# Performance work log

Measured on AMD Instinct MI355X. Metric: run time of the kernel, lower is better.

## Reference

```python
import jax, jax.numpy as jnp
import numpy as np

N_NODES = 100000
N_EDGES = 1600000
D_IN = 128
D_OUT = 128


def setup_inputs() -> dict:
    key = jax.random.key(0)
    k1, k2, k3, k4, k5 = jax.random.split(key, 5)
    h = jax.random.normal(k1, (N_NODES, D_IN), dtype=jnp.float32)
    src = jax.random.randint(k2, (N_EDGES,), 0, N_NODES, dtype=jnp.int64)
    dst = jax.random.randint(k3, (N_EDGES,), 0, N_NODES, dtype=jnp.int64)
    # Glorot-ish init for linear weights (PyTorch nn.Linear style: [out, in])
    scale = 1.0 / np.sqrt(D_IN)
    W_self = jax.random.uniform(k4, (D_OUT, D_IN), jnp.float32, -scale, scale)
    W_neigh = jax.random.uniform(k5, (D_OUT, D_IN), jnp.float32, -scale, scale)
    b = jnp.zeros((D_OUT,), dtype=jnp.float32)
    return {"h": h, "src": src, "dst": dst, "W_self": W_self,
            "W_neigh": W_neigh, "b": b}


def reference(h, src, dst, W_self, W_neigh, b):
    n_nodes = h.shape[0]
    # neighbor gather + segment-mean over in-neighbors (DGL fn.copy_u + fn.mean)
    msg = h[src]                                            # [E, D_in]
    neigh_sum = jax.ops.segment_sum(msg, dst, num_segments=n_nodes)
    deg = jax.ops.segment_sum(jnp.ones_like(dst, dtype=h.dtype), dst,
                              num_segments=n_nodes)         # [N]
    h_neigh = neigh_sum / jnp.maximum(deg, 1.0)[:, None]    # mean; 0 for isolated
    # SAGEConv mean: fc_self(h) + fc_neigh(h_neigh) + bias
    out = h @ W_self.T + h_neigh @ W_neigh.T + b
    return out
```

## Files before the change

### kernel.cpp

```cpp
#include <hip/hip_runtime.h>
#include <stdint.h>

#define NN 100000
#define NE 1600000
#define DD 128
#define NTILES ((NN + 127) / 128)
#define NB 512
#define CHUNK (NE / NB)
#define NBUCK ((NN + 255) / 256)

typedef __bf16 bf16x8 __attribute__((ext_vector_type(8)));
typedef float f32x4 __attribute__((ext_vector_type(4)));
typedef float f32x2 __attribute__((ext_vector_type(2)));

__device__ __forceinline__ unsigned int f2bf2(float a, float b) {
  union { float f; unsigned u; } x, y;
  x.f = a; y.f = b;
  unsigned ua = x.u + (0x7FFFu + ((x.u >> 16) & 1u));
  unsigned ub = y.u + (0x7FFFu + ((y.u >> 16) & 1u));
  return (ua >> 16) | (ub & 0xFFFF0000u);
}

__global__ __launch_bounds__(256) void zero_kernel(int* __restrict__ p) {
  int t = blockIdx.x * 256 + threadIdx.x;
  if (t < 2 * NBUCK) p[t] = 0;
}

__global__ __launch_bounds__(256) void convert_kernel(
    const float4* __restrict__ hp, uint2* __restrict__ h8,
    uint4* __restrict__ hbf, const int* __restrict__ dst,
    int* __restrict__ ghist) {
  __shared__ int lh[NBUCK];
  int t = threadIdx.x, b = blockIdx.x;
  int gid = b * 256 + t;
  float4 a = hp[2 * gid], c = hp[2 * gid + 1];
  int lo = __builtin_amdgcn_cvt_pk_fp8_f32(a.x, a.y, 0, false);
  lo = __builtin_amdgcn_cvt_pk_fp8_f32(a.z, a.w, lo, true);
  int hi = __builtin_amdgcn_cvt_pk_fp8_f32(c.x, c.y, 0, false);
  hi = __builtin_amdgcn_cvt_pk_fp8_f32(c.z, c.w, hi, true);
  h8[gid] = make_uint2((unsigned)lo, (unsigned)hi);

  uint4 q;
  q.x = f2bf2(a.x, a.y);
  q.y = f2bf2(a.z, a.w);
  q.z = f2bf2(c.x, c.y);
  q.w = f2bf2(c.z, c.w);
  int m = t >> 4, c8 = t & 15;
  int rt = b & 7, kc = c8 >> 2, quad = c8 & 3;
  hbf[(size_t)(b >> 3) * 2048 + (((rt << 2) + kc) << 6) + (quad << 4) + m] = q;

  if (b < NB) {
    for (int i = t; i < NBUCK; i += 256) lh[i] = 0;
    __syncthreads();
    int e0 = b * CHUNK;
    for (int e = e0 + t; e < e0 + CHUNK; e += 256)
      atomicAdd(&lh[dst[e] >> 8], 1);
    __syncthreads();
    for (int i = t; i < NBUCK; i += 256)
      if (lh[i]) atomicAdd(&ghist[i], lh[i]);
  }
}

__global__ __launch_bounds__(256) void coarse_scatter_kernel(
    const int* __restrict__ src, const int* __restrict__ dst,
    const int* __restrict__ ghist, int* __restrict__ gcur,
    unsigned* __restrict__ ebuf) {
  __shared__ int lhp[512];
  __shared__ int gbp[512];
  __shared__ int lbase[NBUCK];
  __shared__ int lcur[NBUCK];
  __shared__ int gstart[NBUCK];
  __shared__ unsigned sdata[CHUNK];
  __shared__ int sgpos[CHUNK];
  int t = threadIdx.x, b = blockIdx.x;
  lhp[t] = 0;
  lhp[t + 256] = 0;
  gbp[t] = (t < NBUCK) ? ghist[t] : 0;
  gbp[t + 256] = (t + 256 < NBUCK) ? ghist[t + 256] : 0;
  __syncthreads();
  int e0 = b * CHUNK;
  for (int e = e0 + t; e < e0 + CHUNK; e += 256)
    atomicAdd(&lhp[dst[e] >> 8], 1);
  __syncthreads();
  int c0 = lhp[t], c1 = lhp[t + 256];
  int g0 = gbp[t], g1 = gbp[t + 256];
  for (int d = 1; d < 512; d <<= 1) {
    int x0 = (t >= d) ? lhp[t - d] : 0;
    int x1 = ((t + 256) >= d) ? lhp[t + 256 - d] : 0;
    int y0 = (t >= d) ? gbp[t - d] : 0;
    int y1 = ((t + 256) >= d) ? gbp[t + 256 - d] : 0;
    __syncthreads();
    lhp[t] += x0; lhp[t + 256] += x1;
    gbp[t] += y0; gbp[t + 256] += y1;
    __syncthreads();
  }
  if (t < NBUCK) {
    lbase[t] = lhp[t] - c0;
    lcur[t] = 0;
    int resv = c0 ? atomicAdd(&gcur[t], c0) : 0;
    gstart[t] = (gbp[t] - g0) + resv;
  }
  int i2 = t + 256;
  if (i2 < NBUCK) {
    lbase[i2] = lhp[i2] - c1;
    lcur[i2] = 0;
    int resv = c1 ? atomicAdd(&gcur[i2], c1) : 0;
    gstart[i2] = (gbp[i2] - g1) + resv;
  }
  __syncthreads();
  for (int e = e0 + t; e < e0 + CHUNK; e += 256) {
    int d = dst[e], s = src[e];
    int bk = d >> 8;
    int slot = atomicAdd(&lcur[bk], 1);
    int lp = lbase[bk] + slot;
    sdata[lp] = ((unsigned)(d & 255) << 24) | (unsigned)s;
    sgpos[lp] = gstart[bk] + slot;
  }
  __syncthreads();
  for (int j = t; j < CHUNK; j += 256) ebuf[sgpos[j]] = sdata[j];
}

__global__ __launch_bounds__(256) void fine_sort_kernel(
    const unsigned* __restrict__ ebuf, const int* __restrict__ ghist,
    int* __restrict__ csr, int* __restrict__ offs) {
  __shared__ int gbp[512];
  __shared__ int hist[256], scn[256], cur[256];
  int t = threadIdx.x, g = blockIdx.x;
  gbp[t] = (t < NBUCK) ? ghist[t] : 0;
  gbp[t + 256] = (t + 256 < NBUCK) ? ghist[t + 256] : 0;
  hist[t] = 0;
  __syncthreads();
  for (int d = 1; d < 512; d <<= 1) {
    int y0 = (t >= d) ? gbp[t - d] : 0;
    int y1 = ((t + 256) >= d) ? gbp[t + 256 - d] : 0;
    __syncthreads();
    gbp[t] += y0; gbp[t + 256] += y1;
    __syncthreads();
  }
  int end = gbp[g];
  int base = end - ghist[g];
  for (int j = base + t; j < end; j += 256)
    atomicAdd(&hist[ebuf[j] >> 24], 1);
  __syncthreads();
  int v = hist[t];
  scn[t] = v;
  __syncthreads();
  for (int d = 1; d < 256; d <<= 1) {
    int x = (t >= d) ? scn[t - d] : 0;
    __syncthreads();
    scn[t] += x;
    __syncthreads();
  }
  int excl = scn[t] - v;
  int node = g * 256 + t;
  if (node < NN) offs[node] = base + excl;
  if (node == NN - 1) offs[NN] = NE;
  cur[t] = excl;
  __syncthreads();
  for (int j = base + t; j < end; j += 256) {
    unsigned p = ebuf[j];
    int pos = atomicAdd(&cur[p >> 24], 1);
    csr[base + pos] = (int)(p & 0x00FFFFFFu);
  }
}

__device__ __forceinline__ void acc16(float* a, uint4 u) {
  f32x2 p;
  p = __builtin_amdgcn_cvt_pk_f32_fp8(u.x, false); a[0] += p.x;  a[1] += p.y;
  p = __builtin_amdgcn_cvt_pk_f32_fp8(u.x, true);  a[2] += p.x;  a[3] += p.y;
  p = __builtin_amdgcn_cvt_pk_f32_fp8(u.y, false); a[4] += p.x;  a[5] += p.y;
  p = __builtin_amdgcn_cvt_pk_f32_fp8(u.y, true);  a[6] += p.x;  a[7] += p.y;
  p = __builtin_amdgcn_cvt_pk_f32_fp8(u.z, false); a[8] += p.x;  a[9] += p.y;
  p = __builtin_amdgcn_cvt_pk_f32_fp8(u.z, true);  a[10] += p.x; a[11] += p.y;
  p = __builtin_amdgcn_cvt_pk_f32_fp8(u.w, false); a[12] += p.x; a[13] += p.y;
  p = __builtin_amdgcn_cvt_pk_f32_fp8(u.w, true);  a[14] += p.x; a[15] += p.y;
}

__global__ __launch_bounds__(256) void gather_frag_kernel(
    const uint4* __restrict__ h8, const int* __restrict__ offs,
    const int* __restrict__ csr, uint4* __restrict__ hfrag) {
  int q = (blockIdx.x * 256 + threadIdx.x) >> 3;
  int l = threadIdx.x & 7;
  float a[16];
#pragma unroll
  for (int i = 0; i < 16; i++) a[i] = 0.f;
  float sc = 0.f;
  if (q < NN) {
    int off0 = offs[q], off1 = offs[q + 1];
    int j = off0;
    for (; j + 4 <= off1; j += 4) {
      int s0 = csr[j], s1 = csr[j + 1], s2 = csr[j + 2], s3 = csr[j + 3];
      uint4 u0 = h8[(size_t)s0 * 8 + l];
      uint4 u1 = h8[(size_t)s1 * 8 + l];
      uint4 u2 = h8[(size_t)s2 * 8 + l];
      uint4 u3 = h8[(size_t)s3 * 8 + l];
      acc16(a, u0); acc16(a, u1); acc16(a, u2); acc16(a, u3);
    }
    for (; j < off1; j++) acc16(a, h8[(size_t)csr[j] * 8 + l]);
    int deg = off1 - off0;
    sc = (deg > 0) ? (1.0f / (float)deg) : 0.0f;
  }
  uint4 r0, r1;
  r0.x = f2bf2(a[0] * sc, a[1] * sc);   r0.y = f2bf2(a[2] * sc, a[3] * sc);
  r0.z = f2bf2(a[4] * sc, a[5] * sc);   r0.w = f2bf2(a[6] * sc, a[7] * sc);
  r1.x = f2bf2(a[8] * sc, a[9] * sc);   r1.y = f2bf2(a[10] * sc, a[11] * sc);
  r1.z = f2bf2(a[12] * sc, a[13] * sc); r1.w = f2bf2(a[14] * sc, a[15] * sc);
  int r = q & 127;
  int rt = r >> 4, m = r & 15;
  int kc = l >> 1, quad = (l & 1) << 1;
  int slot = (((rt << 2) + kc) << 6) + (quad << 4) + m;
  uint4* base = hfrag + (size_t)(q >> 7) * 2048;
  base[slot] = r0;
  base[slot + 16] = r1;
}

__device__ __forceinline__ void stage_w(const float* __restrict__ X,
                                        uint4* buf, int t) {
#pragma unroll
  for (int i = 0; i < 8; i++) {
    int id = t + (i << 8);
    int r = id >> 4;
    int c8 = id & 15;
    const float4* p = (const float4*)(X + (size_t)r * DD + (c8 << 3));
    float4 v0 = p[0], v1 = p[1];
    uint4 q;
    q.x = f2bf2(v0.x, v0.y);
    q.y = f2bf2(v0.z, v0.w);
    q.z = f2bf2(v1.x, v1.y);
    q.w = f2bf2(v1.z, v1.w);
    int rt = r >> 4, m = r & 15, kc = c8 >> 2, quad = c8 & 3;
    buf[(((rt << 2) + kc) << 6) + (quad << 4) + m] = q;
  }
}

__device__ __forceinline__ void compute_reg(const uint4* a, const uint4* sWb,
                                            f32x4 acc[2][8], int lane) {
#pragma unroll
  for (int kc = 0; kc < 4; kc++) {
    bf16x8 bfr[8];
#pragma unroll
    for (int n = 0; n < 8; n++)
      bfr[n] = *(const bf16x8*)&sWb[(((n << 2) + kc) << 6) + lane];
    bf16x8 a0 = *(const bf16x8*)&a[kc];
    bf16x8 a1 = *(const bf16x8*)&a[4 + kc];
#pragma unroll
    for (int n = 0; n < 8; n++) {
      acc[0][n] = __builtin_amdgcn_mfma_f32_16x16x32_bf16(a0, bfr[n], acc[0][n], 0, 0, 0);
      acc[1][n] = __builtin_amdgcn_mfma_f32_16x16x32_bf16(a1, bfr[n], acc[1][n], 0, 0, 0);
    }
  }
}

__global__ __launch_bounds__(256, 2) void gemm_kernel(
    const uint4* __restrict__ hbf, const uint4* __restrict__ hfrag,
    const float* __restrict__ Wself, const float* __restrict__ Wneigh,
    const float* __restrict__ bias, float* __restrict__ out) {
  __shared__ uint4 sW[4096];
  int t = threadIdx.x;
  int wv = t >> 6;
  int lane = t & 63;
  int row0 = blockIdx.x * 128;

  const uint4* fb1 = hbf + (size_t)blockIdx.x * 2048;
  const uint4* fb2 = hfrag + (size_t)blockIdx.x * 2048;
  uint4 a1[8], a2[8];
#pragma unroll
  for (int kc = 0; kc < 4; kc++) {
    int s0 = ((((wv * 2 + 0) << 2) + kc) << 6) + lane;
    int s1 = ((((wv * 2 + 1) << 2) + kc) << 6) + lane;
    a1[kc] = fb1[s0]; a1[4 + kc] = fb1[s1];
    a2[kc] = fb2[s0]; a2[4 + kc] = fb2[s1];
  }

  stage_w(Wself, sW, t);
  stage_w(Wneigh, sW + 2048, t);

  f32x4 acc[2][8];
#pragma unroll
  for (int i = 0; i < 2; i++)
#pragma unroll
    for (int n = 0; n < 8; n++) acc[i][n] = f32x4{0.f, 0.f, 0.f, 0.f};

  __syncthreads();
  compute_reg(a1, sW, acc, lane);
  compute_reg(a2, sW + 2048, acc, lane);

  int col = lane & 15, rq = lane >> 4;
  float bv[8];
#pragma unroll
  for (int n = 0; n < 8; n++) bv[n] = bias[n * 16 + col];
#pragma unroll
  for (int rt = 0; rt < 2; rt++) {
    int rb = row0 + (wv * 2 + rt) * 16 + rq * 4;
#pragma unroll
    for (int r = 0; r < 4; r++) {
      int row = rb + r;
      if (row < NN) {
        float* op = out + (size_t)row * DD + col;
#pragma unroll
        for (int n = 0; n < 8; n++) op[n * 16] = acc[rt][n][r] + bv[n];
      }
    }
  }
}

extern "C" void kernel_launch(void* const* d_in, const int* in_sizes, int n_in,
                              void* d_out, int out_size, void* d_ws, size_t ws_size,
                              hipStream_t stream) {
  const float* h      = (const float*)d_in[0];
  const int*   src    = (const int*)d_in[1];
  const int*   dst    = (const int*)d_in[2];
  const float* Wself  = (const float*)d_in[3];
  const float* Wneigh = (const float*)d_in[4];
  const float* bias   = (const float*)d_in[5];
  float* out = (float*)d_out;

  char* ws = (char*)d_ws;
  unsigned* h8       = (unsigned*)ws;
  unsigned* hbf      = (unsigned*)(ws + 12800000);
  unsigned* hfrag    = (unsigned*)(ws + 38424576);
  unsigned* ebuf     = (unsigned*)(ws + 38424576);
  int*      csr      = (int*)(ws + 64049152);
  int*      offs     = (int*)(ws + 70449152);
  int*      ghist    = (int*)(ws + 70849168);
  int*      gcur     = (int*)(ws + 70850732);

  zero_kernel<<<(2 * NBUCK + 255) / 256, 256, 0, stream>>>(ghist);
  convert_kernel<<<6250, 256, 0, stream>>>((const float4*)h, (uint2*)h8,
                                           (uint4*)hbf, dst, ghist);
  coarse_scatter_kernel<<<NB, 256, 0, stream>>>(src, dst, ghist, gcur, ebuf);
  fine_sort_kernel<<<NBUCK, 256, 0, stream>>>(ebuf, ghist, csr, offs);
  gather_frag_kernel<<<(NTILES * 128) / 32, 256, 0, stream>>>(
      (const uint4*)h8, offs, csr, (uint4*)hfrag);
  gemm_kernel<<<NTILES, 256, 0, stream>>>((const uint4*)hbf, (const uint4*)hfrag,
                                          Wself, Wneigh, bias, out);
}
```

Before: 229.5 us.

## Build CSR via per-node atomic counting and scan, shrink GEMM LDS footprint

```diff
diff --git a/kernel.cpp b/kernel.cpp
--- a/kernel.cpp
+++ b/kernel.cpp
@@ -5,9 +5,8 @@
 #define NE 1600000
 #define DD 128
 #define NTILES ((NN + 127) / 128)
-#define NB 512
-#define CHUNK (NE / NB)
 #define NBUCK ((NN + 255) / 256)
+#define NCNT (NBUCK * 256)
 
 typedef __bf16 bf16x8 __attribute__((ext_vector_type(8)));
 typedef float f32x4 __attribute__((ext_vector_type(4)));
@@ -21,16 +20,14 @@
   return (ua >> 16) | (ub & 0xFFFF0000u);
 }
 
-__global__ __launch_bounds__(256) void zero_kernel(int* __restrict__ p) {
-  int t = blockIdx.x * 256 + threadIdx.x;
-  if (t < 2 * NBUCK) p[t] = 0;
+__global__ __launch_bounds__(256) void zero_kernel(int* __restrict__ cnt) {
+  cnt[blockIdx.x * 256 + threadIdx.x] = 0;
 }
 
 __global__ __launch_bounds__(256) void convert_kernel(
     const float4* __restrict__ hp, uint2* __restrict__ h8,
     uint4* __restrict__ hbf, const int* __restrict__ dst,
-    int* __restrict__ ghist) {
-  __shared__ int lh[NBUCK];
+    int* __restrict__ cnt) {
   int t = threadIdx.x, b = blockIdx.x;
   int gid = b * 256 + t;
   float4 a = hp[2 * gid], c = hp[2 * gid + 1];
@@ -49,119 +46,67 @@
   int rt = b & 7, kc = c8 >> 2, quad = c8 & 3;
   hbf[(size_t)(b >> 3) * 2048 + (((rt << 2) + kc) << 6) + (quad << 4) + m] = q;
 
-  if (b < NB) {
-    for (int i = t; i < NBUCK; i += 256) lh[i] = 0;
-    __syncthreads();
-    int e0 = b * CHUNK;
-    for (int e = e0 + t; e < e0 + CHUNK; e += 256)
-      atomicAdd(&lh[dst[e] >> 8], 1);
-    __syncthreads();
-    for (int i = t; i < NBUCK; i += 256)
-      if (lh[i]) atomicAdd(&ghist[i], lh[i]);
-  }
-}
-
-__global__ __launch_bounds__(256) void coarse_scatter_kernel(
-    const int* __restrict__ src, const int* __restrict__ dst,
-    const int* __restrict__ ghist, int* __restrict__ gcur,
-    unsigned* __restrict__ ebuf) {
-  __shared__ int lhp[512];
-  __shared__ int gbp[512];
-  __shared__ int lbase[NBUCK];
-  __shared__ int lcur[NBUCK];
-  __shared__ int gstart[NBUCK];
-  __shared__ unsigned sdata[CHUNK];
-  __shared__ int sgpos[CHUNK];
-  int t = threadIdx.x, b = blockIdx.x;
-  lhp[t] = 0;
-  lhp[t + 256] = 0;
-  gbp[t] = (t < NBUCK) ? ghist[t] : 0;
-  gbp[t + 256] = (t + 256 < NBUCK) ? ghist[t + 256] : 0;
-  __syncthreads();
-  int e0 = b * CHUNK;
-  for (int e = e0 + t; e < e0 + CHUNK; e += 256)
-    atomicAdd(&lhp[dst[e] >> 8], 1);
-  __syncthreads();
-  int c0 = lhp[t], c1 = lhp[t + 256];
-  int g0 = gbp[t], g1 = gbp[t + 256];
+  atomicAdd(&cnt[dst[gid]], 1);
+}
+
+__global__ __launch_bounds__(256) void blocksum_kernel(const int* __restrict__ cnt,
+                                                       int* __restrict__ bsum) {
+  __shared__ int s[256];
+  int t = threadIdx.x;
+  s[t] = cnt[blockIdx.x * 256 + t];
+  __syncthreads();
+  for (int d = 128; d > 0; d >>= 1) {
+    if (t < d) s[t] += s[t + d];
+    __syncthreads();
+  }
+  if (t == 0) bsum[blockIdx.x] = s[0];
+}
+
+__global__ __launch_bounds__(512) void scanbsum_kernel(const int* __restrict__ bsum,
+                                                       int* __restrict__ bsum_ex) {
+  __shared__ int s[512];
+  int t = threadIdx.x;
+  int v = (t < NBUCK) ? bsum[t] : 0;
+  s[t] = v;
+  __syncthreads();
   for (int d = 1; d < 512; d <<= 1) {
-    int x0 = (t >= d) ? lhp[t - d] : 0;
-    int x1 = ((t + 256) >= d) ? lhp[t + 256 - d] : 0;
-    int y0 = (t >= d) ? gbp[t - d] : 0;
-    int y1 = ((t + 256) >= d) ? gbp[t + 256 - d] : 0;
-    __syncthreads();
-    lhp[t] += x0; lhp[t + 256] += x1;
-    gbp[t] += y0; gbp[t + 256] += y1;
-    __syncthreads();
-  }
-  if (t < NBUCK) {
-    lbase[t] = lhp[t] - c0;
-    lcur[t] = 0;
-    int resv = c0 ? atomicAdd(&gcur[t], c0) : 0;
-    gstart[t] = (gbp[t] - g0) + resv;
-  }
-  int i2 = t + 256;
-  if (i2 < NBUCK) {
-    lbase[i2] = lhp[i2] - c1;
-    lcur[i2] = 0;
-    int resv = c1 ? atomicAdd(&gcur[i2], c1) : 0;
-    gstart[i2] = (gbp[i2] - g1) + resv;
-  }
-  __syncthreads();
-  for (int e = e0 + t; e < e0 + CHUNK; e += 256) {
-    int d = dst[e], s = src[e];
-    int bk = d >> 8;
-    int slot = atomicAdd(&lcur[bk], 1);
-    int lp = lbase[bk] + slot;
-    sdata[lp] = ((unsigned)(d & 255) << 24) | (unsigned)s;
-    sgpos[lp] = gstart[bk] + slot;
-  }
-  __syncthreads();
-  for (int j = t; j < CHUNK; j += 256) ebuf[sgpos[j]] = sdata[j];
-}
-
-__global__ __launch_bounds__(256) void fine_sort_kernel(
-    const unsigned* __restrict__ ebuf, const int* __restrict__ ghist,
-    int* __restrict__ csr, int* __restrict__ offs) {
-  __shared__ int gbp[512];
-  __shared__ int hist[256], scn[256], cur[256];
-  int t = threadIdx.x, g = blockIdx.x;
-  gbp[t] = (t < NBUCK) ? ghist[t] : 0;
-  gbp[t + 256] = (t + 256 < NBUCK) ? ghist[t + 256] : 0;
-  hist[t] = 0;
-  __syncthreads();
-  for (int d = 1; d < 512; d <<= 1) {
-    int y0 = (t >= d) ? gbp[t - d] : 0;
-    int y1 = ((t + 256) >= d) ? gbp[t + 256 - d] : 0;
-    __syncthreads();
-    gbp[t] += y0; gbp[t + 256] += y1;
-    __syncthreads();
-  }
-  int end = gbp[g];
-  int base = end - ghist[g];
-  for (int j = base + t; j < end; j += 256)
-    atomicAdd(&hist[ebuf[j] >> 24], 1);
-  __syncthreads();
-  int v = hist[t];
-  scn[t] = v;
+    int x = (t >= d) ? s[t - d] : 0;
+    __syncthreads();
+    s[t] += x;
+    __syncthreads();
+  }
+  if (t < NBUCK) bsum_ex[t] = s[t] - v;
+}
+
+__global__ __launch_bounds__(256) void scanapply_kernel(const int* __restrict__ cnt,
+                                                        const int* __restrict__ bsum_ex,
+                                                        int* __restrict__ offs,
+                                                        int* __restrict__ cur) {
+  __shared__ int s[256];
+  int t = threadIdx.x;
+  int idx = blockIdx.x * 256 + t;
+  int v = cnt[idx];
+  s[t] = v;
   __syncthreads();
   for (int d = 1; d < 256; d <<= 1) {
-    int x = (t >= d) ? scn[t - d] : 0;
-    __syncthreads();
-    scn[t] += x;
-    __syncthreads();
-  }
-  int excl = scn[t] - v;
-  int node = g * 256 + t;
-  if (node < NN) offs[node] = base + excl;
-  if (node == NN - 1) offs[NN] = NE;
-  cur[t] = excl;
-  __syncthreads();
-  for (int j = base + t; j < end; j += 256) {
-    unsigned p = ebuf[j];
-    int pos = atomicAdd(&cur[p >> 24], 1);
-    csr[base + pos] = (int)(p & 0x00FFFFFFu);
-  }
+    int x = (t >= d) ? s[t - d] : 0;
+    __syncthreads();
+    s[t] += x;
+    __syncthreads();
+  }
+  int excl = bsum_ex[blockIdx.x] + s[t] - v;
+  if (idx < NN) { offs[idx] = excl; cur[idx] = excl; }
+  if (idx == NN - 1) offs[NN] = NE;
+}
+
+__global__ __launch_bounds__(256) void scatter_kernel(const int* __restrict__ src,
+                                                      const int* __restrict__ dst,
+                                                      int* __restrict__ cur,
+                                                      int* __restrict__ csr) {
+  int e = blockIdx.x * 256 + threadIdx.x;
+  int d = dst[e];
+  int pos = atomicAdd(&cur[d], 1);
+  csr[pos] = src[e];
 }
 
 __device__ __forceinline__ void acc16(float* a, uint4 u) {
@@ -251,11 +196,11 @@
   }
 }
 
-__global__ __launch_bounds__(256, 2) void gemm_kernel(
+__global__ __launch_bounds__(256, 4) void gemm_kernel(
     const uint4* __restrict__ hbf, const uint4* __restrict__ hfrag,
     const float* __restrict__ Wself, const float* __restrict__ Wneigh,
     const float* __restrict__ bias, float* __restrict__ out) {
-  __shared__ uint4 sW[4096];
+  __shared__ uint4 sW[2048];
   int t = threadIdx.x;
   int wv = t >> 6;
   int lane = t & 63;
@@ -272,18 +217,19 @@
     a2[kc] = fb2[s0]; a2[4 + kc] = fb2[s1];
   }
 
+  f32x4 acc[2][8];
+#pragma unroll
+  for (int i = 0; i < 2; i++)
+#pragma unroll
+    for (int n = 0; n < 8; n++) acc[i][n] = f32x4{0.f, 0.f, 0.f, 0.f};
+
   stage_w(Wself, sW, t);
-  stage_w(Wneigh, sW + 2048, t);
-
-  f32x4 acc[2][8];
-#pragma unroll
-  for (int i = 0; i < 2; i++)
-#pragma unroll
-    for (int n = 0; n < 8; n++) acc[i][n] = f32x4{0.f, 0.f, 0.f, 0.f};
-
   __syncthreads();
   compute_reg(a1, sW, acc, lane);
-  compute_reg(a2, sW + 2048, acc, lane);
+  __syncthreads();
+  stage_w(Wneigh, sW, t);
+  __syncthreads();
+  compute_reg(a2, sW, acc, lane);
 
   int col = lane & 15, rq = lane >> 4;
   float bv[8];
@@ -319,17 +265,20 @@
   unsigned* h8       = (unsigned*)ws;
   unsigned* hbf      = (unsigned*)(ws + 12800000);
   unsigned* hfrag    = (unsigned*)(ws + 38424576);
-  unsigned* ebuf     = (unsigned*)(ws + 38424576);
   int*      csr      = (int*)(ws + 64049152);
   int*      offs     = (int*)(ws + 70449152);
-  int*      ghist    = (int*)(ws + 70849168);
-  int*      gcur     = (int*)(ws + 70850732);
-
-  zero_kernel<<<(2 * NBUCK + 255) / 256, 256, 0, stream>>>(ghist);
+  int*      cnt      = (int*)(ws + 70849168);
+  int*      cur      = (int*)(ws + 71249552);
+  int*      bsum     = (int*)(ws + 71649936);
+  int*      bsum_ex  = (int*)(ws + 71651504);
+
+  zero_kernel<<<NBUCK, 256, 0, stream>>>(cnt);
   convert_kernel<<<6250, 256, 0, stream>>>((const float4*)h, (uint2*)h8,
-                                           (uint4*)hbf, dst, ghist);
-  coarse_scatter_kernel<<<NB, 256, 0, stream>>>(src, dst, ghist, gcur, ebuf);
-  fine_sort_kernel<<<NBUCK, 256, 0, stream>>>(ebuf, ghist, csr, offs);
+                                           (uint4*)hbf, dst, cnt);
+  blocksum_kernel<<<NBUCK, 256, 0, stream>>>(cnt, bsum);
+  scanbsum_kernel<<<1, 512, 0, stream>>>(bsum, bsum_ex);
+  scanapply_kernel<<<NBUCK, 256, 0, stream>>>(cnt, bsum_ex, offs, cur);
+  scatter_kernel<<<6250, 256, 0, stream>>>(src, dst, cur, csr);
   gather_frag_kernel<<<(NTILES * 128) / 32, 256, 0, stream>>>(
       (const uint4*)h8, offs, csr, (uint4*)hfrag);
   gemm_kernel<<<NTILES, 256, 0, stream>>>((const uint4*)hbf, (const uint4*)hfrag,
```

Result: slower. 365.1 us (+59.1%).

## Fuse fine bucket sort into neighbor gather via shared memory; halve GEMM LDS

Applied to the files above, without the earlier changes.

```diff
diff --git a/kernel.cpp b/kernel.cpp
--- a/kernel.cpp
+++ b/kernel.cpp
@@ -8,6 +8,7 @@
 #define NB 512
 #define CHUNK (NE / NB)
 #define NBUCK ((NN + 255) / 256)
+#define MAXBE 6144
 
 typedef __bf16 bf16x8 __attribute__((ext_vector_type(8)));
 typedef float f32x4 __attribute__((ext_vector_type(4)));
@@ -120,50 +121,6 @@
   for (int j = t; j < CHUNK; j += 256) ebuf[sgpos[j]] = sdata[j];
 }
 
-__global__ __launch_bounds__(256) void fine_sort_kernel(
-    const unsigned* __restrict__ ebuf, const int* __restrict__ ghist,
-    int* __restrict__ csr, int* __restrict__ offs) {
-  __shared__ int gbp[512];
-  __shared__ int hist[256], scn[256], cur[256];
-  int t = threadIdx.x, g = blockIdx.x;
-  gbp[t] = (t < NBUCK) ? ghist[t] : 0;
-  gbp[t + 256] = (t + 256 < NBUCK) ? ghist[t + 256] : 0;
-  hist[t] = 0;
-  __syncthreads();
-  for (int d = 1; d < 512; d <<= 1) {
-    int y0 = (t >= d) ? gbp[t - d] : 0;
-    int y1 = ((t + 256) >= d) ? gbp[t + 256 - d] : 0;
-    __syncthreads();
-    gbp[t] += y0; gbp[t + 256] += y1;
-    __syncthreads();
-  }
-  int end = gbp[g];
-  int base = end - ghist[g];
-  for (int j = base + t; j < end; j += 256)
-    atomicAdd(&hist[ebuf[j] >> 24], 1);
-  __syncthreads();
-  int v = hist[t];
-  scn[t] = v;
-  __syncthreads();
-  for (int d = 1; d < 256; d <<= 1) {
-    int x = (t >= d) ? scn[t - d] : 0;
-    __syncthreads();
-    scn[t] += x;
-    __syncthreads();
-  }
-  int excl = scn[t] - v;
-  int node = g * 256 + t;
-  if (node < NN) offs[node] = base + excl;
-  if (node == NN - 1) offs[NN] = NE;
-  cur[t] = excl;
-  __syncthreads();
-  for (int j = base + t; j < end; j += 256) {
-    unsigned p = ebuf[j];
-    int pos = atomicAdd(&cur[p >> 24], 1);
-    csr[base + pos] = (int)(p & 0x00FFFFFFu);
-  }
-}
-
 __device__ __forceinline__ void acc16(float* a, uint4 u) {
   f32x2 p;
   p = __builtin_amdgcn_cvt_pk_f32_fp8(u.x, false); a[0] += p.x;  a[1] += p.y;
@@ -176,42 +133,84 @@
   p = __builtin_amdgcn_cvt_pk_f32_fp8(u.w, true);  a[14] += p.x; a[15] += p.y;
 }
 
-__global__ __launch_bounds__(256) void gather_frag_kernel(
-    const uint4* __restrict__ h8, const int* __restrict__ offs,
-    const int* __restrict__ csr, uint4* __restrict__ hfrag) {
-  int q = (blockIdx.x * 256 + threadIdx.x) >> 3;
-  int l = threadIdx.x & 7;
-  float a[16];
-#pragma unroll
-  for (int i = 0; i < 16; i++) a[i] = 0.f;
-  float sc = 0.f;
-  if (q < NN) {
-    int off0 = offs[q], off1 = offs[q + 1];
-    int j = off0;
-    for (; j + 4 <= off1; j += 4) {
-      int s0 = csr[j], s1 = csr[j + 1], s2 = csr[j + 2], s3 = csr[j + 3];
+__global__ __launch_bounds__(256) void gather_bucket_kernel(
+    const unsigned* __restrict__ ebuf, const int* __restrict__ ghist,
+    const uint4* __restrict__ h8, uint4* __restrict__ hfrag) {
+  __shared__ int gbp[512];
+  __shared__ int hist[256], st[256], cur[256];
+  __shared__ int ssort[MAXBE];
+  int t = threadIdx.x;
+  int bid = blockIdx.x;
+  int g = bid >> 1, p = bid & 1;
+  gbp[t] = (t < NBUCK) ? ghist[t] : 0;
+  gbp[t + 256] = (t + 256 < NBUCK) ? ghist[t + 256] : 0;
+  hist[t] = 0;
+  __syncthreads();
+  for (int d = 1; d < 512; d <<= 1) {
+    int y0 = (t >= d) ? gbp[t - d] : 0;
+    int y1 = ((t + 256) >= d) ? gbp[t + 256 - d] : 0;
+    __syncthreads();
+    gbp[t] += y0; gbp[t + 256] += y1;
+    __syncthreads();
+  }
+  int end = gbp[g];
+  int base = end - ghist[g];
+  for (int j = base + t; j < end; j += 256)
+    atomicAdd(&hist[ebuf[j] >> 24], 1);
+  __syncthreads();
+  int deg = hist[t];
+  st[t] = deg;
+  __syncthreads();
+  for (int d = 1; d < 256; d <<= 1) {
+    int x = (t >= d) ? st[t - d] : 0;
+    __syncthreads();
+    st[t] += x;
+    __syncthreads();
+  }
+  int start = st[t] - deg;
+  __syncthreads();
+  st[t] = start;
+  cur[t] = start;
+  __syncthreads();
+  for (int j = base + t; j < end; j += 256) {
+    unsigned e = ebuf[j];
+    int pos = atomicAdd(&cur[e >> 24], 1);
+    ssort[pos] = (int)(e & 0x00FFFFFFu);
+  }
+  __syncthreads();
+  int grp = t >> 3, l = t & 7;
+#pragma unroll 1
+  for (int k = 0; k < 4; k++) {
+    int r = grp * 4 + k;
+    int ln = p * 128 + r;
+    int j = st[ln];
+    int jend = j + hist[ln];
+    float a[16];
+#pragma unroll
+    for (int i = 0; i < 16; i++) a[i] = 0.f;
+    for (; j + 4 <= jend; j += 4) {
+      int s0 = ssort[j], s1 = ssort[j + 1], s2 = ssort[j + 2], s3 = ssort[j + 3];
       uint4 u0 = h8[(size_t)s0 * 8 + l];
       uint4 u1 = h8[(size_t)s1 * 8 + l];
       uint4 u2 = h8[(size_t)s2 * 8 + l];
       uint4 u3 = h8[(size_t)s3 * 8 + l];
       acc16(a, u0); acc16(a, u1); acc16(a, u2); acc16(a, u3);
     }
-    for (; j < off1; j++) acc16(a, h8[(size_t)csr[j] * 8 + l]);
-    int deg = off1 - off0;
-    sc = (deg > 0) ? (1.0f / (float)deg) : 0.0f;
-  }
-  uint4 r0, r1;
-  r0.x = f2bf2(a[0] * sc, a[1] * sc);   r0.y = f2bf2(a[2] * sc, a[3] * sc);
-  r0.z = f2bf2(a[4] * sc, a[5] * sc);   r0.w = f2bf2(a[6] * sc, a[7] * sc);
-  r1.x = f2bf2(a[8] * sc, a[9] * sc);   r1.y = f2bf2(a[10] * sc, a[11] * sc);
-  r1.z = f2bf2(a[12] * sc, a[13] * sc); r1.w = f2bf2(a[14] * sc, a[15] * sc);
-  int r = q & 127;
-  int rt = r >> 4, m = r & 15;
-  int kc = l >> 1, quad = (l & 1) << 1;
-  int slot = (((rt << 2) + kc) << 6) + (quad << 4) + m;
-  uint4* base = hfrag + (size_t)(q >> 7) * 2048;
-  base[slot] = r0;
-  base[slot + 16] = r1;
+    for (; j < jend; j++) acc16(a, h8[(size_t)ssort[j] * 8 + l]);
+    int dg = hist[ln];
+    float sc = (dg > 0) ? (1.0f / (float)dg) : 0.0f;
+    uint4 r0, r1;
+    r0.x = f2bf2(a[0] * sc, a[1] * sc);   r0.y = f2bf2(a[2] * sc, a[3] * sc);
+    r0.z = f2bf2(a[4] * sc, a[5] * sc);   r0.w = f2bf2(a[6] * sc, a[7] * sc);
+    r1.x = f2bf2(a[8] * sc, a[9] * sc);   r1.y = f2bf2(a[10] * sc, a[11] * sc);
+    r1.z = f2bf2(a[12] * sc, a[13] * sc); r1.w = f2bf2(a[14] * sc, a[15] * sc);
+    int rt = r >> 4, m = r & 15;
+    int kc = l >> 1, quad = (l & 1) << 1;
+    int slot = (((rt << 2) + kc) << 6) + (quad << 4) + m;
+    uint4* bp = hfrag + (size_t)bid * 2048;
+    bp[slot] = r0;
+    bp[slot + 16] = r1;
+  }
 }
 
 __device__ __forceinline__ void stage_w(const float* __restrict__ X,
@@ -251,11 +250,11 @@
   }
 }
 
-__global__ __launch_bounds__(256, 2) void gemm_kernel(
+__global__ __launch_bounds__(256, 4) void gemm_kernel(
     const uint4* __restrict__ hbf, const uint4* __restrict__ hfrag,
     const float* __restrict__ Wself, const float* __restrict__ Wneigh,
     const float* __restrict__ bias, float* __restrict__ out) {
-  __shared__ uint4 sW[4096];
+  __shared__ uint4 sW[2048];
   int t = threadIdx.x;
   int wv = t >> 6;
   int lane = t & 63;
@@ -272,18 +271,19 @@
     a2[kc] = fb2[s0]; a2[4 + kc] = fb2[s1];
   }
 
+  f32x4 acc[2][8];
+#pragma unroll
+  for (int i = 0; i < 2; i++)
+#pragma unroll
+    for (int n = 0; n < 8; n++) acc[i][n] = f32x4{0.f, 0.f, 0.f, 0.f};
+
   stage_w(Wself, sW, t);
-  stage_w(Wneigh, sW + 2048, t);
-
-  f32x4 acc[2][8];
-#pragma unroll
-  for (int i = 0; i < 2; i++)
-#pragma unroll
-    for (int n = 0; n < 8; n++) acc[i][n] = f32x4{0.f, 0.f, 0.f, 0.f};
-
   __syncthreads();
   compute_reg(a1, sW, acc, lane);
-  compute_reg(a2, sW + 2048, acc, lane);
+  __syncthreads();
+  stage_w(Wneigh, sW, t);
+  __syncthreads();
+  compute_reg(a2, sW, acc, lane);
 
   int col = lane & 15, rq = lane >> 4;
   float bv[8];
@@ -319,19 +319,16 @@
   unsigned* h8       = (unsigned*)ws;
   unsigned* hbf      = (unsigned*)(ws + 12800000);
   unsigned* hfrag    = (unsigned*)(ws + 38424576);
-  unsigned* ebuf     = (unsigned*)(ws + 38424576);
-  int*      csr      = (int*)(ws + 64049152);
-  int*      offs     = (int*)(ws + 70449152);
-  int*      ghist    = (int*)(ws + 70849168);
-  int*      gcur     = (int*)(ws + 70850732);
-
-  zero_kernel<<<(2 * NBUCK + 255) / 256, 256, 0, stream>>>(ghist);
+  unsigned* ebuf     = (unsigned*)(ws + 64049152);
+  int*      ghist    = (int*)(ws + 70449152);
+  int*      gcur     = (int*)(ws + 70450716);
+
+  zero_kernel<<<4, 256, 0, stream>>>(ghist);
   convert_kernel<<<6250, 256, 0, stream>>>((const float4*)h, (uint2*)h8,
                                            (uint4*)hbf, dst, ghist);
   coarse_scatter_kernel<<<NB, 256, 0, stream>>>(src, dst, ghist, gcur, ebuf);
-  fine_sort_kernel<<<NBUCK, 256, 0, stream>>>(ebuf, ghist, csr, offs);
-  gather_frag_kernel<<<(NTILES * 128) / 32, 256, 0, stream>>>(
-      (const uint4*)h8, offs, csr, (uint4*)hfrag);
+  gather_bucket_kernel<<<NTILES, 256, 0, stream>>>(ebuf, ghist,
+                                                   (const uint4*)h8, (uint4*)hfrag);
   gemm_kernel<<<NTILES, 256, 0, stream>>>((const uint4*)hbf, (const uint4*)hfrag,
                                           Wself, Wneigh, bias, out);
 }
```

After: 239.2 us. +4.3%, slower.
